# Performance work log

Measured on AMD Instinct MI355X. Metric: run time of the kernel, lower is better.

The kernel has to match this reference:

```python
import jax, jax.numpy as jnp
import numpy as np

N, K, C, H, V = 4096, 32, 128, 128, 21   # residues, kNN, node/edge dim, hidden, vocab
NEG_SLOPE = 0.2

def gatv2(src_feat, tgt_feat, edge_feat, Wl, bl, Wr, br, We, be, att, b_out):
    # GATv2Conv (1 head, eval mode) on a regular kNN graph.
    # src_feat: [N,K,Din] gathered source-node features per edge; tgt_feat: [N,Din]
    xl = src_feat @ Wl + bl                       # [N,K,C]
    xr = tgt_feat @ Wr + br                       # [N,C]
    ee = edge_feat @ We + be                      # [N,K,C]
    m = jax.nn.leaky_relu(xl + xr[:, None, :] + ee, NEG_SLOPE)
    alpha = jax.nn.softmax(jnp.einsum('nkc,c->nk', m, att), axis=1)
    return jnp.einsum('nk,nkc->nc', alpha, xl) + b_out

def setup_inputs():
    key = jax.random.key(0)
    ks = jax.random.split(key, 32)
    w = lambda k, s: jax.random.normal(k, s, jnp.float32) * 0.05
    z0 = lambda s: jnp.zeros(s, jnp.float32)
    return dict(
        E=jax.random.normal(ks[0], (N, K, C), jnp.float32),
        E_idx=jax.random.randint(ks[1], (N, K), 0, N),
        S=jax.random.randint(ks[2], (N,), 0, V),
        mask=jnp.ones((N,), jnp.float32),
        chain_M=jnp.ones((N,), jnp.float32),
        z=jax.random.normal(ks[3], (N,), jnp.float32),
        Wl1=w(ks[4], (C, C)), bl1=z0((C,)),
        Wr1=w(ks[5], (C, C)), br1=z0((C,)),
        We1=w(ks[6], (C, C)), be1=z0((C,)),
        a1=w(ks[7], (C,)), bo1=z0((C,)),
        Wl2=w(ks[8], (C + H, C)), bl2=z0((C,)),
        Wr2=w(ks[9], (C + H, C)), br2=z0((C,)),
        We2=w(ks[10], (C, C)), be2=z0((C,)),
        a2=w(ks[11], (C,)), bo2=z0((C,)),
        W_s=w(ks[12], (V, H)),
        W_out=w(ks[13], (C, V)), b_out=z0((V,)),
    )

def reference(E, E_idx, S, mask, chain_M, z,
              Wl1, bl1, Wr1, br1, We1, be1, a1, bo1,
              Wl2, bl2, Wr2, br2, We2, be2, a2, bo2,
              W_s, W_out, b_out):
    # encoder GAT over zero-initialized node features
    x0 = jnp.zeros((N, C), E.dtype)
    node_attr = gatv2(x0[E_idx], x0, E, Wl1, bl1, Wr1, br1, We1, be1, a1, bo1)
    seq_attr = W_s[S]                                        # [N,H]
    h_full = jnp.concatenate([node_attr, seq_attr], -1)      # [N,C+H]
    h_mask = jnp.concatenate([node_attr, jnp.zeros_like(seq_attr)], -1)
    cm = chain_M * mask
    decoding_order = jnp.argsort((cm + 1e-4) * jnp.abs(z))   # [N]
    P = jax.nn.one_hot(decoding_order, N, dtype=E.dtype)     # [N,N] permutation
    L = 1.0 - jnp.triu(jnp.ones((N, N), E.dtype))            # strictly lower tri
    order_mask_backward = jnp.einsum('ij,iq,jp->qp', L, P, P)
    mask_attend = jnp.take_along_axis(order_mask_backward, E_idx, axis=1)[..., None]
    m1d = mask[:, None, None]
    mask_bw = m1d * mask_attend
    mask_fw = m1d * (1.0 - mask_attend)
    # per-edge source features: neighbor seq embedding visible only if decoded earlier
    src = h_full[E_idx] * mask_bw + h_mask[E_idx] * mask_fw  # [N,K,C+H]
    out = gatv2(src, h_mask, E, Wl2, bl2, Wr2, br2, We2, be2, a2, bo2)
    logits = out @ W_out + b_out
    return jax.nn.log_softmax(logits, axis=-1)
```

## Files before the change

kernel.cpp:

```cpp
#include <hip/hip_runtime.h>
#include <hip/hip_bf16.h>

typedef short short8 __attribute__((ext_vector_type(8)));
typedef float float4v __attribute__((ext_vector_type(4)));

#define WS_T   0
#define WS_D   2688
#define WS_C   2816
#define WS_A2  3072
#define WS_G   7296
#define WS_B0  7744
#define WS_B1  7776
#define WS_M   7808

__device__ __forceinline__ unsigned int pack2bf(float a, float b) {
  union { float f; unsigned int u; } xa, xb;
  xa.f = a; xb.f = b;
  return ((xa.u + 0x8000u) >> 16) | ((xb.u + 0x8000u) & 0xFFFF0000u);
}

__global__ __launch_bounds__(256) void pg14_pre(
    const float* __restrict__ Wl2, const float* __restrict__ Wr2,
    const float* __restrict__ We2, const float* __restrict__ bl1,
    const float* __restrict__ bl2, const float* __restrict__ br2,
    const float* __restrict__ be2, const float* __restrict__ a2,
    const float* __restrict__ bo1, const float* __restrict__ bo2,
    const float* __restrict__ W_s, const float* __restrict__ mask,
    const float* __restrict__ chain_M, const float* __restrict__ z,
    const int* __restrict__ S, const float* __restrict__ W_out,
    const float* __restrict__ b_out, void* __restrict__ ws)
{
  __shared__ float sA[128], sB[128], sP[2][128];
  short* wsW = (short*)ws;
  float* F = (float*)ws + 8192;
  const int b = blockIdx.x, tid = threadIdx.x;

  if (b < 64) {
    const int s = b * 256 + tid;
    const int row = s >> 7, c = s & 127;
    const int q = row >> 5, lh = (row & 31) >> 3, j = row & 7;
    const int t = c >> 4, cl = c & 15;
    union { float f; unsigned int u; } x; x.f = We2[s];
    const unsigned int r = x.u + 0x7FFFu + ((x.u >> 16) & 1u);
    wsW[(((q * 8 + t) * 64) + lh * 16 + cl) * 8 + j] = (short)(r >> 16);
  } else if (b < 85) {
    const int v = b - 64;
    const int half = tid >> 7, c = tid & 127;
    float acc = 0.f;
#pragma unroll 8
    for (int h = half * 64; h < half * 64 + 64; h++)
      acc += W_s[v * 128 + h] * Wl2[(128 + h) * 128 + c];
    sP[half][c] = acc;
    __syncthreads();
    if (tid < 128) {
      const float t = sP[0][tid] + sP[1][tid];
      F[WS_T + v * 128 + tid] = t;
      sA[tid] = t;
    }
    __syncthreads();
    if (tid < 42) {
      const int u  = (tid < 21) ? tid : tid - 21;
      const int h2 = (tid < 21) ? 0 : 1;
      float g = 0.f;
      for (int c2 = h2 * 64; c2 < h2 * 64 + 64; c2++)
        g = fmaf(sA[c2], W_out[c2 * 21 + u], g);
      sB[tid] = g;
    }
    __syncthreads();
    if (tid < 21)
      F[WS_G + v * 21 + tid] = sB[tid] + sB[21 + tid];
  } else if (b < 101) {
    const int n = (b - 85) * 256 + tid;
    F[WS_M + 2 * n] = (chain_M[n] * mask[n] + 1e-4f) * fabsf(z[n]);
    ((int*)F)[WS_M + 2 * n + 1] = S[n];
  } else {
    if (tid < 128) {
      const int c = tid;
      float cl0 = 0.f;
#pragma unroll 8
      for (int i = 0; i < 128; i++)
        cl0 += (bl1[i] + bo1[i]) * Wl2[i * 128 + c];
      F[WS_C + c] = cl0;
      sB[c] = cl0;
    } else {
      const int c = tid - 128;
      float cr0 = 0.f;
#pragma unroll 8
      for (int i = 0; i < 128; i++)
        cr0 += (bl1[i] + bo1[i]) * Wr2[i * 128 + c];
      F[WS_D + c]  = be2[c] + bl2[c] + br2[c] + cr0;
      F[WS_A2 + c] = a2[c];
      sA[c] = bl2[c] + bo2[c];
    }
    __syncthreads();
    if (tid < 21) {
      float b0 = b_out[tid];
      for (int c = 0; c < 128; c++)
        b0 = fmaf(sA[c], W_out[c * 21 + tid], b0);
      F[WS_B0 + tid] = b0;
    } else if (tid >= 64 && tid < 85) {
      const int u = tid - 64;
      float b1 = 0.f;
      for (int c = 0; c < 128; c++)
        b1 = fmaf(sB[c], W_out[c * 21 + u], b1);
      F[WS_B1 + u] = b1;
    }
  }
}

__global__ __launch_bounds__(256, 4) void pg14_main(
    const float* __restrict__ E, const int* __restrict__ E_idx,
    const float* __restrict__ mask, const void* __restrict__ ws,
    float* __restrict__ out)
{
  __shared__ __align__(16) short ldsW[16384];

  const short* wsW = (const short*)ws;
  const float* F = (const float*)ws + 8192;
  const int tid  = threadIdx.x;
  const int wave = tid >> 6;
  const int lane = tid & 63;
  const int quad = lane >> 4;
  const int lid  = lane & 15;
  const int n    = blockIdx.x * 4 + wave;
  const float maskn = mask[n];

  int jidx = 0;
  if (lane < 32) jidx = E_idx[n * 32 + lane];

  const float* rowp = E + (size_t)n * 4096 + (size_t)lid * 128 + quad * 8;
  short8 afr[2][4];
#pragma unroll
  for (int g = 0; g < 2; g++)
#pragma unroll
    for (int q = 0; q < 4; q++) {
      const float* p = rowp + g * 2048 + q * 32;
      const float4 A = *(const float4*)p;
      const float4 B = *(const float4*)(p + 4);
      union { short8 s; unsigned int u[4]; } v;
      v.u[0] = pack2bf(A.x, A.y);
      v.u[1] = pack2bf(A.z, A.w);
      v.u[2] = pack2bf(B.x, B.y);
      v.u[3] = pack2bf(B.z, B.w);
      afr[g][q] = v.s;
    }

#pragma unroll
  for (int i = 0; i < 8; i++) {
    const int c = i * 256 + tid;
    *(short8*)(ldsW + c * 8) = *(const short8*)(wsW + c * 8);
  }

  float wkv = 0.f; int rvv = 0;
  const float keyn = F[WS_M + 2 * n];
  if (lane < 32) {
    const float2 mj = *(const float2*)(F + WS_M + 2 * jidx);
    const int before = (mj.x < keyn) || (mj.x == keyn && jidx < n);
    wkv = before ? maskn : 0.f;
    union { float f; int i; } cv; cv.f = mj.y; rvv = cv.i;
  }
  int rows[2][4]; float wks[2][4];
#pragma unroll
  for (int g = 0; g < 2; g++)
#pragma unroll
    for (int r = 0; r < 4; r++) {
      const int kk = g * 16 + quad * 4 + r;
      rows[g][r] = __shfl(rvv, kk) * 128;
      wks[g][r]  = __shfl(wkv, kk);
    }

  float dvt[8], a2t[8];
#pragma unroll
  for (int t = 0; t < 8; t++) {
    const int c = t * 16 + lid;
    dvt[t] = F[WS_D + c] + maskn * F[WS_C + c];
    a2t[t] = F[WS_A2 + c];
  }

  __syncthreads();

  float part[2][4] = {{0.f, 0.f, 0.f, 0.f}, {0.f, 0.f, 0.f, 0.f}};
#pragma unroll
  for (int t = 0; t < 8; t++) {
    short8 bfr[4];
#pragma unroll
    for (int q = 0; q < 4; q++)
      bfr[q] = *(const short8*)(ldsW + (((q * 8 + t) * 64) + lane) * 8);
    float4v ac0 = {0.f, 0.f, 0.f, 0.f}, ac1 = {0.f, 0.f, 0.f, 0.f};
#pragma unroll
    for (int q = 0; q < 4; q++) {
      ac0 = __builtin_amdgcn_mfma_f32_16x16x32_bf16(afr[0][q], bfr[q], ac0, 0, 0, 0);
      ac1 = __builtin_amdgcn_mfma_f32_16x16x32_bf16(afr[1][q], bfr[q], ac1, 0, 0, 0);
    }
    const int c = t * 16 + lid;
#pragma unroll
    for (int r = 0; r < 4; r++) {
      float v0 = ac0[r] + dvt[t] + wks[0][r] * F[WS_T + rows[0][r] + c];
      float v1 = ac1[r] + dvt[t] + wks[1][r] * F[WS_T + rows[1][r] + c];
      v0 = fmaxf(v0, 0.f) + 0.2f * fminf(v0, 0.f);
      v1 = fmaxf(v1, 0.f) + 0.2f * fminf(v1, 0.f);
      part[0][r] = fmaf(v0, a2t[t], part[0][r]);
      part[1][r] = fmaf(v1, a2t[t], part[1][r]);
    }
  }
  float sreg[2][4];
#pragma unroll
  for (int g = 0; g < 2; g++)
#pragma unroll
    for (int r = 0; r < 4; r++) {
      float v = part[g][r];
      v += __shfl_xor(v, 1);
      v += __shfl_xor(v, 2);
      v += __shfl_xor(v, 4);
      v += __shfl_xor(v, 8);
      sreg[g][r] = v;
    }

  float mx = -1e30f;
#pragma unroll
  for (int g = 0; g < 2; g++)
#pragma unroll
    for (int r = 0; r < 4; r++) mx = fmaxf(mx, sreg[g][r]);
  mx = fmaxf(mx, __shfl_xor(mx, 16));
  mx = fmaxf(mx, __shfl_xor(mx, 32));
  float eg[2][4], esum = 0.f;
#pragma unroll
  for (int g = 0; g < 2; g++)
#pragma unroll
    for (int r = 0; r < 4; r++) {
      eg[g][r] = expf(sreg[g][r] - mx);
      esum += eg[g][r];
    }
  esum += __shfl_xor(esum, 16);
  esum += __shfl_xor(esum, 32);
  const float inv = 1.f / esum;
  float cg[2][4];
#pragma unroll
  for (int g = 0; g < 2; g++)
#pragma unroll
    for (int r = 0; r < 4; r++) cg[g][r] = eg[g][r] * inv * wks[g][r];

  float lg = (lane < 21) ? (F[WS_B0 + lane] + maskn * F[WS_B1 + lane]) : -1e30f;
#pragma unroll
  for (int kk = 0; kk < 32; kk++) {
    const int g = kk >> 4, sq = (kk >> 2) & 3, r = kk & 3;
    const float cf = __shfl(cg[g][r], sq * 16);
    const int row = __shfl(rvv, kk) * 21;
    if (lane < 21) lg = fmaf(cf, F[WS_G + row + lane], lg);
  }

  float lmx = lg;
  lmx = fmaxf(lmx, __shfl_xor(lmx, 1));
  lmx = fmaxf(lmx, __shfl_xor(lmx, 2));
  lmx = fmaxf(lmx, __shfl_xor(lmx, 4));
  lmx = fmaxf(lmx, __shfl_xor(lmx, 8));
  lmx = fmaxf(lmx, __shfl_xor(lmx, 16));
  float ex = (lane < 21) ? expf(lg - lmx) : 0.f;
  float es = ex;
  es += __shfl_xor(es, 1);
  es += __shfl_xor(es, 2);
  es += __shfl_xor(es, 4);
  es += __shfl_xor(es, 8);
  es += __shfl_xor(es, 16);
  if (lane < 21)
    out[n * 21 + lane] = lg - lmx - logf(es);
}

extern "C" void kernel_launch(void* const* d_in, const int* in_sizes, int n_in,
                              void* d_out, int out_size, void* d_ws, size_t ws_size,
                              hipStream_t stream)
{
  const float* E       = (const float*)d_in[0];
  const int*   E_idx   = (const int*)d_in[1];
  const int*   S       = (const int*)d_in[2];
  const float* mask    = (const float*)d_in[3];
  const float* chain_M = (const float*)d_in[4];
  const float* z       = (const float*)d_in[5];
  const float* bl1     = (const float*)d_in[7];
  const float* bo1     = (const float*)d_in[13];
  const float* Wl2     = (const float*)d_in[14];
  const float* bl2     = (const float*)d_in[15];
  const float* Wr2     = (const float*)d_in[16];
  const float* br2     = (const float*)d_in[17];
  const float* We2     = (const float*)d_in[18];
  const float* be2     = (const float*)d_in[19];
  const float* a2      = (const float*)d_in[20];
  const float* bo2     = (const float*)d_in[21];
  const float* W_s     = (const float*)d_in[22];
  const float* W_out   = (const float*)d_in[23];
  const float* b_out   = (const float*)d_in[24];

  pg14_pre<<<102, 256, 0, stream>>>(Wl2, Wr2, We2, bl1, bl2, br2, be2, a2,
                                    bo1, bo2, W_s, mask, chain_M, z, S,
                                    W_out, b_out, d_ws);
  pg14_main<<<1024, 256, 0, stream>>>(E, E_idx, mask, d_ws, (float*)d_out);
}
```

Before: 161.3 us.

## Fuse preprocessing into main kernel with global atomic flag barrier

Merges the preprocessing kernel into the main kernel. The first 102 blocks do the precompute roles, then signal completion through an agent-scope atomic counter. Every block spins on that counter after issuing its E loads, which removes one kernel launch and lets the E fetch overlap the precompute. It relies on all 102 role blocks being co-resident or scheduled first, and the flag baseline (flag+1) is read in a way that looks fragile across repeated calls. The per-channel bias and attention values are now loaded inside the loop instead of being hoisted.

```diff
diff --git a/kernel.cpp b/kernel.cpp
--- a/kernel.cpp
+++ b/kernel.cpp
@@ -12,6 +12,8 @@
 #define WS_B0  7744
 #define WS_B1  7776
 #define WS_M   7808
+#define N_ROLE 102
+#define FLAG_BYTE_OFF (1u << 20)
 
 __device__ __forceinline__ unsigned int pack2bf(float a, float b) {
   union { float f; unsigned int u; } xa, xb;
@@ -19,114 +21,114 @@
   return ((xa.u + 0x8000u) >> 16) | ((xb.u + 0x8000u) & 0xFFFF0000u);
 }
 
-__global__ __launch_bounds__(256) void pg14_pre(
+__global__ __launch_bounds__(256, 4) void pg15_fused(
+    const float* __restrict__ E, const int* __restrict__ E_idx,
+    const float* __restrict__ mask, const float* __restrict__ chain_M,
+    const float* __restrict__ z, const int* __restrict__ S,
     const float* __restrict__ Wl2, const float* __restrict__ Wr2,
     const float* __restrict__ We2, const float* __restrict__ bl1,
     const float* __restrict__ bl2, const float* __restrict__ br2,
     const float* __restrict__ be2, const float* __restrict__ a2,
     const float* __restrict__ bo1, const float* __restrict__ bo2,
-    const float* __restrict__ W_s, const float* __restrict__ mask,
-    const float* __restrict__ chain_M, const float* __restrict__ z,
-    const int* __restrict__ S, const float* __restrict__ W_out,
-    const float* __restrict__ b_out, void* __restrict__ ws)
-{
-  __shared__ float sA[128], sB[128], sP[2][128];
-  short* wsW = (short*)ws;
-  float* F = (float*)ws + 8192;
-  const int b = blockIdx.x, tid = threadIdx.x;
-
-  if (b < 64) {
-    const int s = b * 256 + tid;
-    const int row = s >> 7, c = s & 127;
-    const int q = row >> 5, lh = (row & 31) >> 3, j = row & 7;
-    const int t = c >> 4, cl = c & 15;
-    union { float f; unsigned int u; } x; x.f = We2[s];
-    const unsigned int r = x.u + 0x7FFFu + ((x.u >> 16) & 1u);
-    wsW[(((q * 8 + t) * 64) + lh * 16 + cl) * 8 + j] = (short)(r >> 16);
-  } else if (b < 85) {
-    const int v = b - 64;
-    const int half = tid >> 7, c = tid & 127;
-    float acc = 0.f;
-#pragma unroll 8
-    for (int h = half * 64; h < half * 64 + 64; h++)
-      acc += W_s[v * 128 + h] * Wl2[(128 + h) * 128 + c];
-    sP[half][c] = acc;
-    __syncthreads();
-    if (tid < 128) {
-      const float t = sP[0][tid] + sP[1][tid];
-      F[WS_T + v * 128 + tid] = t;
-      sA[tid] = t;
-    }
-    __syncthreads();
-    if (tid < 42) {
-      const int u  = (tid < 21) ? tid : tid - 21;
-      const int h2 = (tid < 21) ? 0 : 1;
-      float g = 0.f;
-      for (int c2 = h2 * 64; c2 < h2 * 64 + 64; c2++)
-        g = fmaf(sA[c2], W_out[c2 * 21 + u], g);
-      sB[tid] = g;
-    }
-    __syncthreads();
-    if (tid < 21)
-      F[WS_G + v * 21 + tid] = sB[tid] + sB[21 + tid];
-  } else if (b < 101) {
-    const int n = (b - 85) * 256 + tid;
-    F[WS_M + 2 * n] = (chain_M[n] * mask[n] + 1e-4f) * fabsf(z[n]);
-    ((int*)F)[WS_M + 2 * n + 1] = S[n];
-  } else {
-    if (tid < 128) {
-      const int c = tid;
-      float cl0 = 0.f;
-#pragma unroll 8
-      for (int i = 0; i < 128; i++)
-        cl0 += (bl1[i] + bo1[i]) * Wl2[i * 128 + c];
-      F[WS_C + c] = cl0;
-      sB[c] = cl0;
-    } else {
-      const int c = tid - 128;
-      float cr0 = 0.f;
-#pragma unroll 8
-      for (int i = 0; i < 128; i++)
-        cr0 += (bl1[i] + bo1[i]) * Wr2[i * 128 + c];
-      F[WS_D + c]  = be2[c] + bl2[c] + br2[c] + cr0;
-      F[WS_A2 + c] = a2[c];
-      sA[c] = bl2[c] + bo2[c];
-    }
-    __syncthreads();
-    if (tid < 21) {
-      float b0 = b_out[tid];
-      for (int c = 0; c < 128; c++)
-        b0 = fmaf(sA[c], W_out[c * 21 + tid], b0);
-      F[WS_B0 + tid] = b0;
-    } else if (tid >= 64 && tid < 85) {
-      const int u = tid - 64;
-      float b1 = 0.f;
-      for (int c = 0; c < 128; c++)
-        b1 = fmaf(sB[c], W_out[c * 21 + u], b1);
-      F[WS_B1 + u] = b1;
-    }
-  }
-}
-
-__global__ __launch_bounds__(256, 4) void pg14_main(
-    const float* __restrict__ E, const int* __restrict__ E_idx,
-    const float* __restrict__ mask, const void* __restrict__ ws,
+    const float* __restrict__ W_s, const float* __restrict__ W_out,
+    const float* __restrict__ b_out, void* __restrict__ ws,
     float* __restrict__ out)
 {
   __shared__ __align__(16) short ldsW[16384];
-
-  const short* wsW = (const short*)ws;
-  const float* F = (const float*)ws + 8192;
-  const int tid  = threadIdx.x;
+  __shared__ float sA[128], sB[128], sP[2][128];
+
+  short* wsW = (short*)ws;
+  float* F = (float*)ws + 8192;
+  unsigned int* flag = (unsigned int*)((char*)ws + FLAG_BYTE_OFF);
+
+  const int b    = blockIdx.x, tid = threadIdx.x;
   const int wave = tid >> 6;
   const int lane = tid & 63;
   const int quad = lane >> 4;
   const int lid  = lane & 15;
-  const int n    = blockIdx.x * 4 + wave;
+  const int n    = b * 4 + wave;
   const float maskn = mask[n];
 
   int jidx = 0;
   if (lane < 32) jidx = E_idx[n * 32 + lane];
+
+  if (b < N_ROLE) {
+    if (b < 64) {
+      const int s = b * 256 + tid;
+      const int row = s >> 7, c = s & 127;
+      const int q = row >> 5, lh = (row & 31) >> 3, j = row & 7;
+      const int t = c >> 4, cl = c & 15;
+      union { float f; unsigned int u; } x; x.f = We2[s];
+      const unsigned int r = x.u + 0x7FFFu + ((x.u >> 16) & 1u);
+      wsW[(((q * 8 + t) * 64) + lh * 16 + cl) * 8 + j] = (short)(r >> 16);
+    } else if (b < 85) {
+      const int v = b - 64;
+      const int half = tid >> 7, c = tid & 127;
+      float acc = 0.f;
+#pragma unroll 8
+      for (int h = half * 64; h < half * 64 + 64; h++)
+        acc += W_s[v * 128 + h] * Wl2[(128 + h) * 128 + c];
+      sP[half][c] = acc;
+      __syncthreads();
+      if (tid < 128) {
+        const float t = sP[0][tid] + sP[1][tid];
+        F[WS_T + v * 128 + tid] = t;
+        sA[tid] = t;
+      }
+      __syncthreads();
+      if (tid < 42) {
+        const int u  = (tid < 21) ? tid : tid - 21;
+        const int h2 = (tid < 21) ? 0 : 1;
+        float g = 0.f;
+        for (int c2 = h2 * 64; c2 < h2 * 64 + 64; c2++)
+          g = fmaf(sA[c2], W_out[c2 * 21 + u], g);
+        sB[tid] = g;
+      }
+      __syncthreads();
+      if (tid < 21)
+        F[WS_G + v * 21 + tid] = sB[tid] + sB[21 + tid];
+    } else if (b < 101) {
+      const int nn = (b - 85) * 256 + tid;
+      F[WS_M + 2 * nn] = (chain_M[nn] * mask[nn] + 1e-4f) * fabsf(z[nn]);
+      ((int*)F)[WS_M + 2 * nn + 1] = S[nn];
+    } else {
+      if (tid < 128) {
+        const int c = tid;
+        float cl0 = 0.f;
+#pragma unroll 8
+        for (int i = 0; i < 128; i++)
+          cl0 += (bl1[i] + bo1[i]) * Wl2[i * 128 + c];
+        F[WS_C + c] = cl0;
+        sB[c] = cl0;
+      } else {
+        const int c = tid - 128;
+        float cr0 = 0.f;
+#pragma unroll 8
+        for (int i = 0; i < 128; i++)
+          cr0 += (bl1[i] + bo1[i]) * Wr2[i * 128 + c];
+        F[WS_D + c]  = be2[c] + bl2[c] + br2[c] + cr0;
+        F[WS_A2 + c] = a2[c];
+        sA[c] = bl2[c] + bo2[c];
+      }
+      __syncthreads();
+      if (tid < 21) {
+        float b0 = b_out[tid];
+        for (int c = 0; c < 128; c++)
+          b0 = fmaf(sA[c], W_out[c * 21 + tid], b0);
+        F[WS_B0 + tid] = b0;
+      } else if (tid >= 64 && tid < 85) {
+        const int u = tid - 64;
+        float b1 = 0.f;
+        for (int c = 0; c < 128; c++)
+          b1 = fmaf(sB[c], W_out[c * 21 + u], b1);
+        F[WS_B1 + u] = b1;
+      }
+    }
+    __syncthreads();
+    if (tid == 0)
+      __hip_atomic_fetch_add(flag, 1u, __ATOMIC_RELEASE,
+                             __HIP_MEMORY_SCOPE_AGENT);
+  }
 
   const float* rowp = E + (size_t)n * 4096 + (size_t)lid * 128 + quad * 8;
   short8 afr[2][4];
@@ -145,6 +147,19 @@
       afr[g][q] = v.s;
     }
 
+  if (tid == 0) {
+    const unsigned int initv =
+        __hip_atomic_load(flag + 1, __ATOMIC_RELAXED, __HIP_MEMORY_SCOPE_AGENT);
+    int guard = 0;
+    while ((unsigned int)(__hip_atomic_load(flag, __ATOMIC_ACQUIRE,
+                              __HIP_MEMORY_SCOPE_AGENT) - initv)
+               < (unsigned int)N_ROLE) {
+      __builtin_amdgcn_s_sleep(2);
+      if (++guard > (1 << 20)) break;
+    }
+  }
+  __syncthreads();
+
 #pragma unroll
   for (int i = 0; i < 8; i++) {
     const int c = i * 256 + tid;
@@ -169,14 +184,6 @@
       wks[g][r]  = __shfl(wkv, kk);
     }
 
-  float dvt[8], a2t[8];
-#pragma unroll
-  for (int t = 0; t < 8; t++) {
-    const int c = t * 16 + lid;
-    dvt[t] = F[WS_D + c] + maskn * F[WS_C + c];
-    a2t[t] = F[WS_A2 + c];
-  }
-
   __syncthreads();
 
   float part[2][4] = {{0.f, 0.f, 0.f, 0.f}, {0.f, 0.f, 0.f, 0.f}};
@@ -193,14 +200,16 @@
       ac1 = __builtin_amdgcn_mfma_f32_16x16x32_bf16(afr[1][q], bfr[q], ac1, 0, 0, 0);
     }
     const int c = t * 16 + lid;
+    const float dvt  = F[WS_D + c] + maskn * F[WS_C + c];
+    const float a2vt = F[WS_A2 + c];
 #pragma unroll
     for (int r = 0; r < 4; r++) {
-      float v0 = ac0[r] + dvt[t] + wks[0][r] * F[WS_T + rows[0][r] + c];
-      float v1 = ac1[r] + dvt[t] + wks[1][r] * F[WS_T + rows[1][r] + c];
+      float v0 = ac0[r] + dvt + wks[0][r] * F[WS_T + rows[0][r] + c];
+      float v1 = ac1[r] + dvt + wks[1][r] * F[WS_T + rows[1][r] + c];
       v0 = fmaxf(v0, 0.f) + 0.2f * fminf(v0, 0.f);
       v1 = fmaxf(v1, 0.f) + 0.2f * fminf(v1, 0.f);
-      part[0][r] = fmaf(v0, a2t[t], part[0][r]);
-      part[1][r] = fmaf(v1, a2t[t], part[1][r]);
+      part[0][r] = fmaf(v0, a2vt, part[0][r]);
+      part[1][r] = fmaf(v1, a2vt, part[1][r]);
     }
   }
   float sreg[2][4];
@@ -290,8 +299,8 @@
   const float* W_out   = (const float*)d_in[23];
   const float* b_out   = (const float*)d_in[24];
 
-  pg14_pre<<<102, 256, 0, stream>>>(Wl2, Wr2, We2, bl1, bl2, br2, be2, a2,
-                                    bo1, bo2, W_s, mask, chain_M, z, S,
-                                    W_out, b_out, d_ws);
-  pg14_main<<<1024, 256, 0, stream>>>(E, E_idx, mask, d_ws, (float*)d_out);
+  pg15_fused<<<1024, 256, 0, stream>>>(E, E_idx, mask, chain_M, z, S,
+                                       Wl2, Wr2, We2, bl1, bl2, br2, be2,
+                                       a2, bo1, bo2, W_s, W_out, b_out,
+                                       d_ws, (float*)d_out);
 }
```

New measurement: 321.7 us. 99.5% more time.
